# Kernel tuning notes

Measured on AMD Instinct MI355X. Metric: run time of the kernel, lower is better.

The kernel has to match this reference:

```python
import jax, jax.numpy as jnp
import numpy as np

N = 8192
D = 256
E = 262144


def setup_inputs() -> dict:
    key = jax.random.key(0)
    kx, ke = jax.random.split(key)
    x = jax.random.normal(kx, (N, D), dtype=jnp.float32)
    edge_index = jax.random.randint(ke, (2, E), 0, N, dtype=jnp.int64)
    return {"x": x, "edge_index": edge_index}


def reference(x, edge_index):
    n, d = x.shape
    xs = x / (d ** 0.25)
    # per-edge similarity: equivalent to einsum('md,nd->mn')[src, dst] without O(n^2 d)
    src, dst = edge_index[0], edge_index[1]
    vals = jnp.einsum('ed,ed->e', xs[src], xs[dst])
    neg = jnp.finfo(jnp.float32).min
    sim = jnp.full((n, n), neg, dtype=x.dtype)
    sim = sim.at[src, dst].set(vals)
    # logaritmic=False branch: plain double softmax, averaged
    scores0 = jax.nn.softmax(sim, axis=1)                # row softmax
    scores1 = jax.nn.softmax(sim, axis=0)                # col softmax (== softmax(sim.T, -1).T)
    scores = (scores0 + scores1) * 0.5
    return scores, sim
```

## Files before the change

### kernel.cpp

```cpp
#include <hip/hip_runtime.h>
#include <float.h>
#include <math.h>

constexpr int Nn = 8192;
constexpr unsigned BG = 0xFF7F0000u;

typedef unsigned u32x4 __attribute__((ext_vector_type(4)));
typedef float fltx4 __attribute__((ext_vector_type(4)));

__device__ __forceinline__ float clamp01(float f) {
    return fminf(fmaxf(f, 0.0f), 1.0f);
}

__global__ void k0_init(const unsigned* __restrict__ ew, unsigned* __restrict__ flag,
                        float* __restrict__ rowsum, float* __restrict__ colsum) {
    int i = blockIdx.x * 256 + threadIdx.x;
    rowsum[i] = 0.0f;
    colsum[i] = 0.0f;
    if (blockIdx.x == 0) {
        __shared__ unsigned acc;
        if (threadIdx.x == 0) acc = 0u;
        __syncthreads();
        atomicOr(&acc, ew[2 * threadIdx.x + 1]);
        __syncthreads();
        if (threadIdx.x == 0) flag[0] = (acc == 0u) ? 1u : 0u;
    }
}

__device__ __forceinline__ void load_edge(const unsigned* ew, unsigned F, int E, int e,
                                          int& s, int& d) {
    s = (int)(ew[e << F] & (Nn - 1));
    d = (int)(ew[(E << F) + (e << F)] & (Nn - 1));
}

__global__ void k1_fill(u32x4* __restrict__ sim4) {
    int tid = blockIdx.x * 256 + threadIdx.x;
    u32x4 v = {BG, BG, BG, BG};
    __builtin_nontemporal_store(v, &sim4[tid]);
}

__global__ void k2_edges(const float* __restrict__ x, const unsigned* __restrict__ ew,
                         const unsigned* __restrict__ flag, unsigned* __restrict__ sim_u,
                         float* __restrict__ vals,
                         float* __restrict__ rowsum, float* __restrict__ colsum, int E) {
    int e = (blockIdx.x << 2) + (threadIdx.x >> 6);
    if (e >= E) return;
    int lane = threadIdx.x & 63;
    unsigned F = flag[0];
    int s, d;
    load_edge(ew, F, E, e, s, d);
    const float4* xa = (const float4*)x + (((size_t)s) << 6) + lane;
    const float4* xb = (const float4*)x + (((size_t)d) << 6) + lane;
    float4 a = *xa;
    float4 b = *xb;
    float v = a.x * b.x + a.y * b.y + a.z * b.z + a.w * b.w;
    #pragma unroll
    for (int off = 32; off; off >>= 1) v += __shfl_xor(v, off);
    v *= 0.0625f;
    if (lane == 0) {
        vals[e] = v;
        unsigned cell = (unsigned)s * (unsigned)Nn + (unsigned)d;
        unsigned old = atomicExch(&sim_u[cell], __float_as_uint(v));
        if (old == BG) {
            float ev = expf(v);
            atomicAdd(&rowsum[s], ev);
            atomicAdd(&colsum[d], ev);
        }
    }
}

__global__ void k3_stats(const float* __restrict__ rowsum, const float* __restrict__ colsum,
                         float* __restrict__ r_row, float* __restrict__ c_col,
                         float* __restrict__ hr, float* __restrict__ hc) {
    int i = blockIdx.x * 256 + threadIdx.x;
    float sr = rowsum[i];
    float bg = (sr == 0.0f) ? 1.0f : 0.0f;
    float ss = sr + (float)Nn * bg;
    r_row[i] = bg / ss;
    hr[i] = 0.5f / ss;
    sr = colsum[i];
    bg = (sr == 0.0f) ? 1.0f : 0.0f;
    ss = sr + (float)Nn * bg;
    c_col[i] = bg / ss;
    hc[i] = 0.5f / ss;
}

__global__ void k4_fill(fltx4* __restrict__ scores4, const float* __restrict__ r_row,
                        const fltx4* __restrict__ c4) {
    int idx = blockIdx.x * 256 + threadIdx.x;
    int i = idx >> 11;
    float ri = r_row[i];
    fltx4 c = c4[idx & 2047];
    fltx4 o;
    o.x = clamp01(0.5f * (ri + c.x));
    o.y = clamp01(0.5f * (ri + c.y));
    o.z = clamp01(0.5f * (ri + c.z));
    o.w = clamp01(0.5f * (ri + c.w));
    __builtin_nontemporal_store(o, &scores4[idx]);
}

__global__ void k5_scatter(const unsigned* __restrict__ ew, const unsigned* __restrict__ flag,
                           const float* __restrict__ vals,
                           const float* __restrict__ hr, const float* __restrict__ hc,
                           float* __restrict__ scores, int E) {
    int e = blockIdx.x * 256 + threadIdx.x;
    if (e >= E) return;
    unsigned F = flag[0];
    int s, d;
    load_edge(ew, F, E, e, s, d);
    float sc = clamp01(expf(vals[e]) * (hr[s] + hc[d]));
    scores[(size_t)s * Nn + d] = sc;
}

extern "C" void kernel_launch(void* const* d_in, const int* in_sizes, int n_in,
                              void* d_out, int out_size, void* d_ws, size_t ws_size,
                              hipStream_t stream) {
    const float* x = (const float*)d_in[0];
    const unsigned* ew = (const unsigned*)d_in[1];
    const int E = in_sizes[1] / 2;

    float* scores = (float*)d_out;
    float* sim = scores + (size_t)Nn * (size_t)Nn;

    char* w = (char*)d_ws;
    unsigned* flag = (unsigned*)w;  w += 16;
    float* vals = (float*)w;        w += (size_t)E * 4;
    float* rowsum = (float*)w;      w += (size_t)Nn * 4;
    float* colsum = (float*)w;      w += (size_t)Nn * 4;
    float* r_row = (float*)w;       w += (size_t)Nn * 4;
    float* c_col = (float*)w;       w += (size_t)Nn * 4;
    float* hr = (float*)w;          w += (size_t)Nn * 4;
    float* hc = (float*)w;          w += (size_t)Nn * 4;

    constexpr int FILL_BLOCKS = (Nn / 4) * Nn / 256;
    k0_init<<<Nn / 256, 256, 0, stream>>>(ew, flag, rowsum, colsum);
    k1_fill<<<FILL_BLOCKS, 256, 0, stream>>>((u32x4*)sim);
    k2_edges<<<(E + 3) / 4, 256, 0, stream>>>(x, ew, flag, (unsigned*)sim, vals,
                                              rowsum, colsum, E);
    k3_stats<<<Nn / 256, 256, 0, stream>>>(rowsum, colsum, r_row, c_col, hr, hc);
    k4_fill<<<FILL_BLOCKS, 256, 0, stream>>>((fltx4*)scores, r_row, (const fltx4*)c_col);
    k5_scatter<<<(E + 255) / 256, 256, 0, stream>>>(ew, flag, vals, hr, hc, scores, E);
}
```

Measured before the change: 653.9 us.

## Zero scores during sim fill and patch only empty rows and columns

The scores matrix is now zero-filled in the same kernel that fills sim with the background value, and the init kernel is merged into that fill. The later full-matrix scores fill is replaced by row and column fix-up kernels that write only rows or columns with no edges. This removes one full 256MB read-modify pass and fuses launches, but the fix-up for columns uses strided, uncoalesced writes. It relies on a zero background score being correct for rows and columns that have edges.

```diff
diff --git a/kernel.cpp b/kernel.cpp
--- a/kernel.cpp
+++ b/kernel.cpp
@@ -6,17 +6,29 @@
 constexpr unsigned BG = 0xFF7F0000u;
 
 typedef unsigned u32x4 __attribute__((ext_vector_type(4)));
-typedef float fltx4 __attribute__((ext_vector_type(4)));
 
 __device__ __forceinline__ float clamp01(float f) {
     return fminf(fmaxf(f, 0.0f), 1.0f);
 }
 
-__global__ void k0_init(const unsigned* __restrict__ ew, unsigned* __restrict__ flag,
+__device__ __forceinline__ void load_edge(const unsigned* ew, unsigned F, int E, int e,
+                                          int& s, int& d) {
+    s = (int)(ew[e << F] & (Nn - 1));
+    d = (int)(ew[(E << F) + (e << F)] & (Nn - 1));
+}
+
+__global__ void k1_fill(u32x4* __restrict__ sim4, u32x4* __restrict__ scores4,
+                        const unsigned* __restrict__ ew, unsigned* __restrict__ flag,
                         float* __restrict__ rowsum, float* __restrict__ colsum) {
-    int i = blockIdx.x * 256 + threadIdx.x;
-    rowsum[i] = 0.0f;
-    colsum[i] = 0.0f;
+    int tid = blockIdx.x * 256 + threadIdx.x;
+    u32x4 bg = {BG, BG, BG, BG};
+    u32x4 z = {0u, 0u, 0u, 0u};
+    sim4[tid] = bg;
+    scores4[tid] = z;
+    if (tid < Nn) {
+        rowsum[tid] = 0.0f;
+        colsum[tid] = 0.0f;
+    }
     if (blockIdx.x == 0) {
         __shared__ unsigned acc;
         if (threadIdx.x == 0) acc = 0u;
@@ -25,18 +37,6 @@
         __syncthreads();
         if (threadIdx.x == 0) flag[0] = (acc == 0u) ? 1u : 0u;
     }
-}
-
-__device__ __forceinline__ void load_edge(const unsigned* ew, unsigned F, int E, int e,
-                                          int& s, int& d) {
-    s = (int)(ew[e << F] & (Nn - 1));
-    d = (int)(ew[(E << F) + (e << F)] & (Nn - 1));
-}
-
-__global__ void k1_fill(u32x4* __restrict__ sim4) {
-    int tid = blockIdx.x * 256 + threadIdx.x;
-    u32x4 v = {BG, BG, BG, BG};
-    __builtin_nontemporal_store(v, &sim4[tid]);
 }
 
 __global__ void k2_edges(const float* __restrict__ x, const unsigned* __restrict__ ew,
@@ -85,18 +85,21 @@
     hc[i] = 0.5f / ss;
 }
 
-__global__ void k4_fill(fltx4* __restrict__ scores4, const float* __restrict__ r_row,
-                        const fltx4* __restrict__ c4) {
-    int idx = blockIdx.x * 256 + threadIdx.x;
-    int i = idx >> 11;
+__global__ void k4_rowfix(float* __restrict__ scores, const float* __restrict__ r_row,
+                          const float* __restrict__ c_col) {
+    int i = blockIdx.x;
     float ri = r_row[i];
-    fltx4 c = c4[idx & 2047];
-    fltx4 o;
-    o.x = clamp01(0.5f * (ri + c.x));
-    o.y = clamp01(0.5f * (ri + c.y));
-    o.z = clamp01(0.5f * (ri + c.z));
-    o.w = clamp01(0.5f * (ri + c.w));
-    __builtin_nontemporal_store(o, &scores4[idx]);
+    if (ri == 0.0f) return;
+    for (int j = threadIdx.x; j < Nn; j += 256)
+        scores[(size_t)i * Nn + j] = clamp01(0.5f * (ri + c_col[j]));
+}
+__global__ void k4_colfix(float* __restrict__ scores, const float* __restrict__ r_row,
+                          const float* __restrict__ c_col) {
+    int j = blockIdx.x;
+    float cj = c_col[j];
+    if (cj == 0.0f) return;
+    for (int i = threadIdx.x; i < Nn; i += 256)
+        scores[(size_t)i * Nn + j] = clamp01(0.5f * (r_row[i] + cj));
 }
 
 __global__ void k5_scatter(const unsigned* __restrict__ ew, const unsigned* __restrict__ flag,
@@ -133,11 +136,12 @@
     float* hc = (float*)w;          w += (size_t)Nn * 4;
 
     constexpr int FILL_BLOCKS = (Nn / 4) * Nn / 256;
-    k0_init<<<Nn / 256, 256, 0, stream>>>(ew, flag, rowsum, colsum);
-    k1_fill<<<FILL_BLOCKS, 256, 0, stream>>>((u32x4*)sim);
+    k1_fill<<<FILL_BLOCKS, 256, 0, stream>>>((u32x4*)sim, (u32x4*)scores, ew, flag,
+                                             rowsum, colsum);
     k2_edges<<<(E + 3) / 4, 256, 0, stream>>>(x, ew, flag, (unsigned*)sim, vals,
                                               rowsum, colsum, E);
     k3_stats<<<Nn / 256, 256, 0, stream>>>(rowsum, colsum, r_row, c_col, hr, hc);
-    k4_fill<<<FILL_BLOCKS, 256, 0, stream>>>((fltx4*)scores, r_row, (const fltx4*)c_col);
+    k4_rowfix<<<Nn, 256, 0, stream>>>(scores, r_row, c_col);
+    k4_colfix<<<Nn, 256, 0, stream>>>(scores, r_row, c_col);
     k5_scatter<<<(E + 255) / 256, 256, 0, stream>>>(ew, flag, vals, hr, hc, scores, E);
 }
```

New measurement: 650.0 us. No clear change (-0.6%).
